# Optimization experiments

Measured on AMD Instinct MI355X. Metric: run time of the kernel, lower is better.

## Reference

```python
import jax, jax.numpy as jnp
import numpy as np

EPS = 1e-5  # F.layer_norm default eps
H_STEP = 0.1


def double_layer(x, K1, K2):
    # x: [1, Cin, N]; K1: [Cmid, Cin]; K2: [Cout, Cmid]  (1x1 conv1d == matmul)
    x = jnp.einsum('oc,bcn->bon', K1, x)
    # F.layer_norm(x, x.shape): normalize over the whole tensor, no affine
    m = jnp.mean(x)
    v = jnp.mean((x - m) ** 2)
    x = jnp.tanh((x - m) * jax.lax.rsqrt(v + EPS))
    return jnp.einsum('oc,bcn->bon', K2, x)


def setup_inputs() -> dict:
    key = jax.random.key(0)
    ks = jax.random.split(key, 12)
    N = 4096; nNin = 64; nopen = 256; nhid = 256; nNclose = 256
    nlayer = 8; num_output = 1024; E0 = 16 * N
    stdv = 1e-3
    return {
        'xn': jax.random.normal(ks[0], (1, nNin, N), jnp.float32),
        'K1Nopen': jax.random.normal(ks[1], (nopen, nNin), jnp.float32) * stdv,
        'K2Nopen': jax.random.normal(ks[2], (nopen, nopen), jnp.float32) * stdv,
        'KNclose': jax.random.normal(ks[3], (nNclose, nopen), jnp.float32) * stdv,
        'KN1': jax.random.uniform(ks[4], (nlayer, nhid, 2 * nopen), jnp.float32) * stdv,
        'KN2': jax.random.uniform(ks[5], (nlayer, nopen, nhid), jnp.float32) * stdv,
        'lin1_w': jax.random.normal(ks[6], (nopen, nopen), jnp.float32) / np.sqrt(nopen),
        'lin1_b': jnp.zeros((nopen,), jnp.float32),
        'lin2_w': jax.random.normal(ks[7], (num_output, nopen), jnp.float32) / np.sqrt(nopen),
        'lin2_b': jnp.zeros((num_output,), jnp.float32),
        'edge_i': jax.random.randint(ks[8], (E0,), 0, N),
        'edge_j': jax.random.randint(ks[9], (E0,), 0, N),
    }


def reference(xn, K1Nopen, K2Nopen, KNclose, KN1, KN2,
              lin1_w, lin1_b, lin2_w, lin2_b, edge_i, edge_j):
    N = xn.shape[-1]
    # gcn_norm's add_remaining_self_loops: input edge list has no self loops,
    # so append one per node once (fixed shapes; D[i,i] == exp(0) == 1 == fill).
    I = jnp.concatenate([edge_i, jnp.arange(N)])
    J = jnp.concatenate([edge_j, jnp.arange(N)])

    xn = double_layer(xn, K1Nopen, K2Nopen)  # [1, nopen, N]
    nlayers = KN1.shape[0]
    for i in range(nlayers):
        # --- updateGraph: dense pairwise Gaussian affinity, then gcn_norm ---
        f = xn[0]                          # [C, N]
        sq = jnp.sum(f * f, axis=0)        # [N]
        D = jax.nn.relu(sq[None, :] + sq[:, None] - 2.0 * (f.T @ f))  # [N, N]
        D = jnp.exp(-2.0 * (D / jnp.std(D, ddof=1)))
        w = D[I, J]                                          # gather edge affinities
        deg = jax.ops.segment_sum(w, J, num_segments=N)
        dis = jnp.where(deg > 0, jax.lax.rsqrt(deg), 0.0)
        W = dis[I] * w * dis[J]                              # normalized edge weights [E]
        # --- nodeLap = edgeDiv(nodeGrad(xn)) ---
        g = W[None, None, :] * (xn[:, :, I] - xn[:, :, J])   # nodeGrad [1, C, E]
        wg = (W[None, None, :] * g)[0].T                     # [E, C]
        lap = (jax.ops.segment_sum(wg, I, num_segments=N)
               - jax.ops.segment_sum(wg, J, num_segments=N)).T[None]  # [1, C, N]
        dxn = jnp.concatenate([xn, lap], axis=1)             # varlet features [1, 2C, N]
        dxn = double_layer(dxn, KN1[i], KN2[i])              # [1, C, N]
        xn = xn + H_STEP * dxn                               # heat update

    xn = jnp.einsum('oc,bcn->bon', KNclose, xn)[0].T         # [N, nNclose]
    x = jax.nn.elu(xn @ lin1_w.T + lin1_b)
    x = x @ lin2_w.T + lin2_b
    return jax.nn.log_softmax(x, axis=1)                     # [N, num_output]
```

## Files before the change

kernel.cpp:

```cpp
#include <hip/hip_runtime.h>
#include <hip/hip_bf16.h>

#define N_NODES 4096
#define CF      256
#define CIN     64
#define E0_EDGES 65536
#define NLAYER  8
#define NOUT    1024
#define CN      (CF * N_NODES)
#define STD_BLOCKS 64

typedef unsigned short ushort;
typedef __attribute__((ext_vector_type(8))) short s8v;
typedef __attribute__((ext_vector_type(4))) float f4v;

__device__ __forceinline__ ushort f2bf(float x){
  unsigned int u = __builtin_bit_cast(unsigned int, x);
  return (ushort)((u + 0x7FFFu + ((u >> 16) & 1u)) >> 16);
}
__device__ __forceinline__ float bf2f(ushort h){
  unsigned int u = ((unsigned int)h) << 16;
  return __builtin_bit_cast(float, u);
}

__device__ __forceinline__ float waveSumF(float v){
  #pragma unroll
  for (int o = 32; o; o >>= 1) v += __shfl_xor(v, o);
  return v;
}
__device__ __forceinline__ double waveSumD(double v){
  #pragma unroll
  for (int o = 32; o; o >>= 1) v += __shfl_xor(v, o);
  return v;
}
__device__ __forceinline__ float waveMaxF(float v){
  #pragma unroll
  for (int o = 32; o; o >>= 1) v = fmaxf(v, __shfl_xor(v, o));
  return v;
}
__device__ float blockSumF(float v){
  __shared__ float sm[4];
  v = waveSumF(v);
  int l = threadIdx.x & 63, w = threadIdx.x >> 6;
  __syncthreads();
  if (l == 0) sm[w] = v;
  __syncthreads();
  return sm[0] + sm[1] + sm[2] + sm[3];
}
__device__ double blockSumD(double v){
  __shared__ double sm[4];
  v = waveSumD(v);
  int l = threadIdx.x & 63, w = threadIdx.x >> 6;
  __syncthreads();
  if (l == 0) sm[w] = v;
  __syncthreads();
  return sm[0] + sm[1] + sm[2] + sm[3];
}
__device__ float blockMaxF(float v){
  __shared__ float sm[4];
  v = waveMaxF(v);
  int l = threadIdx.x & 63, w = threadIdx.x >> 6;
  __syncthreads();
  if (l == 0) sm[w] = v;
  __syncthreads();
  return fmaxf(fmaxf(sm[0], sm[1]), fmaxf(sm[2], sm[3]));
}

#define MF(a,b,c) c = __builtin_amdgcn_mfma_f32_16x16x32_bf16(a, b, c, 0, 0, 0)

template<int BK, int NT, int ACT, bool WF32, bool WBF, bool WFH, bool MV, bool TRI>
__global__ __launch_bounds__(256)
void gemmB1(const ushort* __restrict__ A1, const ushort* __restrict__ A2,
            int lda, int splitAt,
            const ushort* __restrict__ B, int ldb,
            float* __restrict__ Cf, ushort* __restrict__ Cb, ushort* __restrict__ Cfh,
            int ldc, size_t cStrideZ, int kChunk,
            float alpha, float beta, const float* __restrict__ bias,
            double* __restrict__ pS, double* __restrict__ pS2)
{
  constexpr int BR  = (NT == 64) ? 64 : 32;
  constexpr int NCA = BK / 32;
  constexpr int NCB = (NT == 64) ? BK / 32 : BK / 64;
  __shared__ ushort As[2][64][BK + 8], Bs[2][BR][BK + 8];
  const int tid = threadIdx.x;
  const int ar = tid >> 2, ak = (tid & 3) * (BK / 4);
  const int br = (NT == 64) ? (tid >> 2) : (tid >> 3);
  const int bk_ = (NT == 64) ? ak : (tid & 7) * (BK / 8);
  int bx = blockIdx.x, by = blockIdx.y;
  if (TRI) {
    const int trT[10] = {0,0,0,0,1,1,1,2,2,3};
    const int tcT[10] = {0,1,2,3,1,2,3,2,3,3};
    by = trT[blockIdx.x]; bx = tcT[blockIdx.x];
  }
  const int row0 = by * 64, col0 = bx * NT;
  const int kStart = blockIdx.z * kChunk;
  const int nT = kChunk / BK;

  const int wid = tid >> 6, lane = tid & 63;
  const int wr = (wid >> 1) * 32, wc = (wid & 1) * (NT / 2);
  const int fr = lane & 15, fk = (lane >> 4) * 8;

  f4v acc[2][NT / 32] = {};
  s8v rA0[NCA], rB0[NCB], rA1[NCA], rB1[NCB];

#define LOADTILE(T, RA, RB) { \
    int k0 = kStart + (T) * BK; \
    const ushort* Ag; int kk; \
    if (k0 < splitAt) { Ag = A1; kk = k0; } else { Ag = A2; kk = k0 - splitAt; } \
    size_t aoff = (size_t)(row0 + ar) * lda + kk + ak; \
    size_t boff = (size_t)(col0 + br) * ldb + k0 + bk_; \
    _Pragma("unroll") \
    for (int c = 0; c < NCA; c++) RA[c] = *(const s8v*)(Ag + aoff + 8 * c); \
    _Pragma("unroll") \
    for (int c = 0; c < NCB; c++) RB[c] = *(const s8v*)(B + boff + 8 * c); }

#define STORETILE(BUF, RA, RB) { \
    _Pragma("unroll") \
    for (int c = 0; c < NCA; c++) *(s8v*)&As[BUF][ar][ak + 8 * c] = RA[c]; \
    _Pragma("unroll") \
    for (int c = 0; c < NCB; c++) *(s8v*)&Bs[BUF][br][bk_ + 8 * c] = RB[c]; }

#define MFMAT(BUF) { \
    _Pragma("unroll") \
    for (int ks = 0; ks < BK; ks += 32) { \
      s8v a0 = *(const s8v*)&As[BUF][wr + fr][ks + fk]; \
      s8v a1 = *(const s8v*)&As[BUF][wr + 16 + fr][ks + fk]; \
      s8v b0 = *(const s8v*)&Bs[BUF][wc + fr][ks + fk]; \
      MF(a0, b0, acc[0][0]); \
      MF(a1, b0, acc[1][0]); \
      if constexpr (NT == 64) { \
        s8v b1 = *(const s8v*)&Bs[BUF][wc + 16 + fr][ks + fk]; \
        MF(a0, b1, acc[0][1]); \
        MF(a1, b1, acc[1][1]); } } }

  LOADTILE(0, rA0, rB0);
  if (nT > 1) LOADTILE(1, rA1, rB1);
  STORETILE(0, rA0, rB0);

  for (int t = 0; t < nT; t += 2) {
    __syncthreads();
    if (t + 2 < nT) LOADTILE(t + 2, rA0, rB0);
    MFMAT(0);
    if (t + 1 < nT) {
      STORETILE(1, rA1, rB1);
      __syncthreads();
      if (t + 3 < nT) LOADTILE(t + 3, rA1, rB1);
      MFMAT(1);
      if (t + 2 < nT) STORETILE(0, rA0, rB0);
    }
  }
#undef LOADTILE
#undef STORETILE
#undef MFMAT

  double s = 0, s2 = 0;
  #pragma unroll
  for (int m = 0; m < 2; m++)
    #pragma unroll
    for (int n = 0; n < NT / 32; n++) {
      const int rowb = row0 + wr + m * 16 + (lane >> 4) * 4;
      const int col  = col0 + wc + n * 16 + fr;
      ushort4 hv;
      #pragma unroll
      for (int q = 0; q < 4; q++) {
        size_t cidx = (size_t)(rowb + q) * ldc + col;
        float v = alpha * acc[m][n][q];
        if (cStrideZ) {
          Cf[blockIdx.z * cStrideZ + cidx] = v;
        } else {
          if (beta != 0.0f) v += beta * Cf[cidx];
          if (bias) v += bias[col];
          if (ACT == 1) v = (v > 0.0f) ? v : expm1f(v);
          if (WF32) Cf[cidx] = v;
          if (WBF)  Cb[cidx] = f2bf(v);
          if (WFH)  ((ushort*)&hv)[q] = f2bf(v);
          if (MV)   { s += v; s2 += (double)v * v; }
        }
      }
      if (WFH && !cStrideZ)
        *(ushort4*)(Cfh + (size_t)col * N_NODES + rowb) = hv;
    }
  if (MV) {
    s  = blockSumD(s);
    s2 = blockSumD(s2);
    if (tid == 0) {
      int bid = blockIdx.y * gridDim.x + blockIdx.x;
      pS[bid] = s; pS2[bid] = s2;
    }
  }
}

#define OFF_K1   0
#define OFF_K2   16384
#define OFF_KNC  81920
#define OFF_KN1  147456
#define OFF_KN2  1196032
#define OFF_L1   1720320
#define OFF_L2   1785856
#define NW_TOT   2048000

__global__ __launch_bounds__(256)
void prepWK(const float* s0, const float* s1, const float* s2, const float* s3,
            const float* s4, const float* s5, const float* s6,
            ushort* __restrict__ h)
{
  const int sizes[7] = {16384, 65536, 65536, 1048576, 524288, 65536, 262144};
  const int offs[7]  = {OFF_K1, OFF_K2, OFF_KNC, OFF_KN1, OFF_KN2, OFF_L1, OFF_L2};
  int seg = blockIdx.y;
  const float* src = seg==0?s0: seg==1?s1: seg==2?s2: seg==3?s3: seg==4?s4: seg==5?s5: s6;
  int n = sizes[seg], off = offs[seg];
  for (int i = blockIdx.x * 256 + threadIdx.x; i < n; i += gridDim.x * 256)
    h[off + i] = f2bf(src[i]);
}

__global__ __launch_bounds__(256)
void transposeBF(const float* __restrict__ in, ushort* __restrict__ outh, int R, int Cc)
{
  __shared__ float t[32][33];
  int x  = blockIdx.x * 32 + threadIdx.x;
  int y0 = blockIdx.y * 32;
  for (int dy = threadIdx.y; dy < 32; dy += 8)
    t[dy][threadIdx.x] = in[(size_t)(y0 + dy) * Cc + x];
  __syncthreads();
  int ox  = y0 + threadIdx.x;
  int oy0 = blockIdx.x * 32;
  for (int dy = threadIdx.y; dy < 32; dy += 8)
    outh[(size_t)(oy0 + dy) * R + ox] = f2bf(t[threadIdx.x][dy]);
}

__global__ __launch_bounds__(256)
void tanhNormBF(ushort* __restrict__ h, const double* __restrict__ pS,
                const double* __restrict__ pS2)
{
  __shared__ float bc[2];
  double a = pS[threadIdx.x] + pS[threadIdx.x + 256];
  double b = pS2[threadIdx.x] + pS2[threadIdx.x + 256];
  a = blockSumD(a);
  b = blockSumD(b);
  if (threadIdx.x == 0) {
    double m   = a / (double)CN;
    double var = b / (double)CN - m * m;
    bc[0] = (float)m;
    bc[1] = (float)(1.0 / sqrt(var + 1e-5));
  }
  __syncthreads();
  float mf = bc[0], rs = bc[1];
  for (size_t i = ((size_t)blockIdx.x * 256 + threadIdx.x) * 8; i < CN;
       i += (size_t)256 * 256 * 8) {
    s8v hv = *(s8v*)(h + i);
    #pragma unroll
    for (int k = 0; k < 8; k++) {
      float x = bf2f((ushort)hv[k]);
      x = tanhf((x - mf) * rs);
      hv[k] = (short)f2bf(x);
    }
    *(s8v*)(h + i) = hv;
  }
}

__global__ __launch_bounds__(256)
void sqSHK(const ushort* __restrict__ fTh, float* __restrict__ sq,
           float* __restrict__ sP, float* __restrict__ hP, float* __restrict__ deg)
{
  __shared__ float smS[4][256], smH[4][256];
  int b = blockIdx.x, w = threadIdx.x >> 6, lane = threadIdx.x & 63;
  if (threadIdx.x < 64) deg[b * 64 + threadIdx.x] = 0.0f;
  float sA[4] = {0,0,0,0}, hA[4] = {0,0,0,0};
  for (int rr = 0; rr < 16; rr++) {
    int n = b * 64 + rr * 4 + w;
    ushort4 u = ((const ushort4*)(fTh + (size_t)n * CF))[lane];
    float x0 = bf2f(u.x), x1 = bf2f(u.y), x2 = bf2f(u.z), x3 = bf2f(u.w);
    float q = waveSumF(x0*x0 + x1*x1 + x2*x2 + x3*x3);
    if (lane == 0) sq[n] = q;
    sA[0] += x0; sA[1] += x1; sA[2] += x2; sA[3] += x3;
    hA[0] += x0*q; hA[1] += x1*q; hA[2] += x2*q; hA[3] += x3*q;
  }
  #pragma unroll
  for (int k = 0; k < 4; k++) { smS[w][lane*4+k] = sA[k]; smH[w][lane*4+k] = hA[k]; }
  __syncthreads();
  int t = threadIdx.x;
  sP[(size_t)b * 256 + t] = smS[0][t] + smS[1][t] + smS[2][t] + smS[3][t];
  hP[(size_t)b * 256 + t] = smH[0][t] + smH[1][t] + smH[2][t] + smH[3][t];
}

__global__ __launch_bounds__(256)
void stdPartsK(const float* __restrict__ sP, const float* __restrict__ hP,
               const float* __restrict__ Gp, const float* __restrict__ sq,
               double* __restrict__ parts)
{
  int b = blockIdx.x, t = threadIdx.x;
  double S1 = 0, S2 = 0, sd = 0, hd = 0, gf = 0;
  for (int i = b * 256 + t; i < N_NODES; i += STD_BLOCKS * 256) {
    double q = sq[i]; S1 += q; S2 += q * q;
  }
  if (b == 0) {
    float sv = 0, hv = 0;
    for (int p = 0; p < 64; p++) { sv += sP[p * 256 + t]; hv += hP[p * 256 + t]; }
    sd = (double)sv * sv; hd = (double)hv * sv;
  }
  for (int i = b * 256 + t; i < CF * CF; i += STD_BLOCKS * 256) {
    int r = i >> 8, c = i & 255;
    if (r > c) continue;
    double g = 0;
    #pragma unroll 4
    for (int z = 0; z < 16; z++) g += Gp[(size_t)z * 65536 + i];
    gf += (r == c) ? g * g : 2.0 * g * g;
  }
  S1 = blockSumD(S1);
  S2 = blockSumD(S2);
  sd = blockSumD(sd);
  hd = blockSumD(hd);
  gf = blockSumD(gf);
  if (t == 0) {
    parts[0 * STD_BLOCKS + b] = S1;
    parts[1 * STD_BLOCKS + b] = S2;
    parts[2 * STD_BLOCKS + b] = sd;
    parts[3 * STD_BLOCKS + b] = hd;
    parts[4 * STD_BLOCKS + b] = gf;
  }
}

__global__ __launch_bounds__(256)
void edgeWK(const int* __restrict__ ei, const int* __restrict__ ej,
            const ushort* __restrict__ fTh, const float* __restrict__ sq,
            const double* __restrict__ parts, float* __restrict__ wE,
            float* __restrict__ deg)
{
  __shared__ float c0s;
  if (threadIdx.x < 64) {
    int l = threadIdx.x;
    double v0 = waveSumD(parts[0 * STD_BLOCKS + l]);
    double v1 = waveSumD(parts[1 * STD_BLOCKS + l]);
    double v2 = waveSumD(parts[2 * STD_BLOCKS + l]);
    double v3 = waveSumD(parts[3 * STD_BLOCKS + l]);
    double v4 = waveSumD(parts[4 * STD_BLOCKS + l]);
    if (l == 0) {
      double NN = (double)N_NODES;
      double sum1 = 2.0 * NN * v0 - 2.0 * v2;
      double sum2 = 2.0 * NN * v1 + 2.0 * v0 * v0 + 4.0 * v4 - 8.0 * v3;
      double n2 = NN * NN;
      double var = (sum2 - sum1 * sum1 / n2) / (n2 - 1.0);
      double sdev = sqrt(var > 0 ? var : 0);
      c0s = (float)(-2.0 / sdev);
    }
  }
  __syncthreads();
  float c0 = c0s;
  int w = threadIdx.x >> 6, lane = threadIdx.x & 63;
  int e0 = (blockIdx.x * 4 + w) * 4;
  for (int q = 0; q < 4; q++) {
    int e = e0 + q;
    int i = ei[e], j = ej[e];
    ushort4 ua = ((const ushort4*)(fTh + (size_t)i * CF))[lane];
    ushort4 ub = ((const ushort4*)(fTh + (size_t)j * CF))[lane];
    float d = waveSumF(bf2f(ua.x)*bf2f(ub.x) + bf2f(ua.y)*bf2f(ub.y) +
                       bf2f(ua.z)*bf2f(ub.z) + bf2f(ua.w)*bf2f(ub.w));
    if (lane == 0) {
      float dist = fmaxf(sq[i] + sq[j] - 2.0f * d, 0.0f);
      float ww = expf(c0 * dist);
      wE[e] = ww;
      unsafeAtomicAdd(&deg[j], ww);
    }
  }
}

__global__ __launch_bounds__(256)
void csrCountK(const int* __restrict__ ei, const int* __restrict__ ej,
               int* __restrict__ cntO, int* __restrict__ cntI)
{
  int e = blockIdx.x * 256 + threadIdx.x;
  atomicAdd(&cntO[ei[e]], 1);
  atomicAdd(&cntI[ej[e]], 1);
}

__global__ __launch_bounds__(256)
void csrScanK(const int* __restrict__ cntO, const int* __restrict__ cntI,
              int* __restrict__ ofsO, int* __restrict__ ofsI)
{
  __shared__ int smO[256], smI[256];
  int t = threadIdx.x;
  int lo[16], li[16];
  int sO = 0, sI = 0;
  #pragma unroll
  for (int k = 0; k < 16; k++) {
    lo[k] = cntO[t * 16 + k]; li[k] = cntI[t * 16 + k];
    sO += lo[k]; sI += li[k];
  }
  smO[t] = sO; smI[t] = sI;
  __syncthreads();
  for (int off = 1; off < 256; off <<= 1) {
    int aO = (t >= off) ? smO[t - off] : 0;
    int aI = (t >= off) ? smI[t - off] : 0;
    __syncthreads();
    smO[t] += aO; smI[t] += aI;
    __syncthreads();
  }
  int bO = smO[t] - sO;
  int bI = smI[t] - sI;
  #pragma unroll
  for (int k = 0; k < 16; k++) {
    ofsO[t * 16 + k] = bO; bO += lo[k];
    ofsI[t * 16 + k] = bI; bI += li[k];
  }
}

__global__ __launch_bounds__(256)
void csrFillK(const int* __restrict__ ei, const int* __restrict__ ej,
              const int* __restrict__ ofsO, const int* __restrict__ ofsI,
              int* __restrict__ curO, int* __restrict__ curI,
              int2* __restrict__ lstO, int2* __restrict__ lstI)
{
  int e = blockIdx.x * 256 + threadIdx.x;
  int i = ei[e], j = ej[e];
  int p = atomicAdd(&curO[i], 1); lstO[ofsO[i] + p] = make_int2(j, e);
  int q = atomicAdd(&curI[j], 1); lstI[ofsI[j] + q] = make_int2(i, e);
}

__global__ __launch_bounds__(256)
void gatherLapK(const int2* __restrict__ lstO, const int2* __restrict__ lstI,
                const int* __restrict__ ofsO, const int* __restrict__ ofsI,
                const int* __restrict__ cntO, const int* __restrict__ cntI,
                const float* __restrict__ wE, const float* __restrict__ deg,
                const ushort* __restrict__ fTh, ushort* __restrict__ lapTh)
{
  int w = threadIdx.x >> 6, lane = threadIdx.x & 63;
  int n = blockIdx.x * 4 + w;
  ushort4 u = ((const ushort4*)(fTh + (size_t)n * CF))[lane];
  float o0 = bf2f(u.x), o1 = bf2f(u.y), o2 = bf2f(u.z), o3 = bf2f(u.w);
  float dn = rsqrtf(1.0f + deg[n]);
  float a0 = 0, a1 = 0, a2 = 0, a3 = 0;
  int p0 = ofsO[n], pc = cntO[n];
  for (int k = 0; k < pc; k++) {
    int2 oe = lstO[p0 + k];
    float W = dn * wE[oe.y] * rsqrtf(1.0f + deg[oe.x]);
    float W2 = W * W;
    ushort4 v = ((const ushort4*)(fTh + (size_t)oe.x * CF))[lane];
    a0 += W2 * (o0 - bf2f(v.x)); a1 += W2 * (o1 - bf2f(v.y));
    a2 += W2 * (o2 - bf2f(v.z)); a3 += W2 * (o3 - bf2f(v.w));
  }
  int q0 = ofsI[n], qc = cntI[n];
  for (int k = 0; k < qc; k++) {
    int2 oe = lstI[q0 + k];
    float W = dn * wE[oe.y] * rsqrtf(1.0f + deg[oe.x]);
    float W2 = W * W;
    ushort4 v = ((const ushort4*)(fTh + (size_t)oe.x * CF))[lane];
    a0 += W2 * (o0 - bf2f(v.x)); a1 += W2 * (o1 - bf2f(v.y));
    a2 += W2 * (o2 - bf2f(v.z)); a3 += W2 * (o3 - bf2f(v.w));
  }
  ushort4 rv;
  rv.x = f2bf(a0); rv.y = f2bf(a1); rv.z = f2bf(a2); rv.w = f2bf(a3);
  ((ushort4*)(lapTh + (size_t)n * CF))[lane] = rv;
}

__global__ __launch_bounds__(256)
void logSoftmaxK(const float* __restrict__ logits, float* __restrict__ out)
{
  int n = blockIdx.x;
  const float* row = logits + (size_t)n * NOUT;
  float mx = -1e30f;
  for (int o = threadIdx.x; o < NOUT; o += 256) mx = fmaxf(mx, row[o]);
  mx = blockMaxF(mx);
  float se = 0;
  for (int o = threadIdx.x; o < NOUT; o += 256) se += expf(row[o] - mx);
  se = blockSumF(se);
  float lse = mx + logf(se);
  for (int o = threadIdx.x; o < NOUT; o += 256) out[(size_t)n * NOUT + o] = row[o] - lse;
}

extern "C" void kernel_launch(void* const* d_in, const int* in_sizes, int n_in,
                              void* d_out, int out_size, void* d_ws, size_t ws_size,
                              hipStream_t stream)
{
  (void)in_sizes; (void)n_in; (void)out_size; (void)ws_size;
  const float* x0      = (const float*)d_in[0];
  const float* K1      = (const float*)d_in[1];
  const float* K2      = (const float*)d_in[2];
  const float* KNclose = (const float*)d_in[3];
  const float* KN1     = (const float*)d_in[4];
  const float* KN2     = (const float*)d_in[5];
  const float* lin1w   = (const float*)d_in[6];
  const float* lin1b   = (const float*)d_in[7];
  const float* lin2w   = (const float*)d_in[8];
  const float* lin2b   = (const float*)d_in[9];
  const int*   ei      = (const int*)d_in[10];
  const int*   ej      = (const int*)d_in[11];
  float* out = (float*)d_out;

  float* base   = (float*)d_ws;
  float* fT     = base;
  float* logits = fT + (size_t)CN;
  float* Gp     = logits + 4 * (size_t)CN;
  float* sq     = Gp + (size_t)CN;
  float* deg    = sq + N_NODES;
  float* sP     = deg + N_NODES;
  float* hP     = sP + 64 * 256;
  float* wE     = hP + 64 * 256;
  double* pS    = (double*)(wE + E0_EDGES + 2);
  double* pS2   = pS + 512;
  double* parts = pS2 + 512;

  ushort* u0 = (ushort*)(((uintptr_t)(parts + 5 * STD_BLOCKS) + 15) & ~(uintptr_t)15);
  ushort* fTh   = u0;
  ushort* fh    = fTh + (size_t)CN;
  ushort* lapTh = fh + (size_t)CN;
  ushort* uTh   = lapTh + (size_t)CN;
  ushort* wH    = uTh + (size_t)CN;
  int* ib = (int*)(((uintptr_t)(wH + NW_TOT) + 15) & ~(uintptr_t)15);
  int*  cntO = ib;
  int*  cntI = cntO + N_NODES;
  int*  ofsO = cntI + N_NODES;
  int*  ofsI = ofsO + N_NODES;
  int*  curO = ofsI + N_NODES;
  int*  curI = curO + N_NODES;
  int2* lstO = (int2*)(curI + N_NODES);
  int2* lstI = lstO + E0_EDGES;

  prepWK<<<dim3(64, 7), 256, 0, stream>>>(K1, K2, KNclose, KN1, KN2, lin1w, lin2w, wH);
  hipMemsetAsync(cntO, 0, 6 * N_NODES * sizeof(int), stream);
  csrCountK<<<E0_EDGES/256, 256, 0, stream>>>(ei, ej, cntO, cntI);
  csrScanK<<<1, 256, 0, stream>>>(cntO, cntI, ofsO, ofsI);
  csrFillK<<<E0_EDGES/256, 256, 0, stream>>>(ei, ej, ofsO, ofsI, curO, curI, lstO, lstI);

  transposeBF<<<dim3(N_NODES/32, CIN/32), dim3(32, 8), 0, stream>>>(x0, fh, CIN, N_NODES);
  gemmB1<64,32,0,0,1,0,1,false><<<dim3(8,64,1), 256, 0, stream>>>(
      fh, fh, CIN, 1 << 30, wH + OFF_K1, CIN,
      nullptr, uTh, nullptr, CF, 0, CIN, 1.f, 0.f, nullptr, pS, pS2);
  tanhNormBF<<<256, 256, 0, stream>>>(uTh, pS, pS2);
  gemmB1<128,32,0,1,1,1,0,false><<<dim3(8,64,1), 256, 0, stream>>>(
      uTh, uTh, CF, 1 << 30, wH + OFF_K2, CF,
      fT, fTh, fh, CF, 0, CF, 1.f, 0.f, nullptr, nullptr, nullptr);

  for (int L = 0; L < NLAYER; L++) {
    const ushort* k1h = wH + OFF_KN1 + (size_t)L * CF * 2 * CF;
    const ushort* k2h = wH + OFF_KN2 + (size_t)L * CF * CF;

    sqSHK<<<64, 256, 0, stream>>>(fTh, sq, sP, hP, deg);
    gemmB1<128,64,0,1,0,0,0,true><<<dim3(10,1,16), 256, 0, stream>>>(
        fh, fh, N_NODES, 1 << 30, fh, N_NODES,
        Gp, nullptr, nullptr, CF, 65536, 256, 1.f, 0.f, nullptr, nullptr, nullptr);
    stdPartsK<<<STD_BLOCKS, 256, 0, stream>>>(sP, hP, Gp, sq, parts);
    edgeWK<<<E0_EDGES/16, 256, 0, stream>>>(ei, ej, fTh, sq, parts, wE, deg);
    gatherLapK<<<N_NODES/4, 256, 0, stream>>>(lstO, lstI, ofsO, ofsI, cntO, cntI,
                                              wE, deg, fTh, lapTh);
    gemmB1<128,32,0,0,1,0,1,false><<<dim3(8,64,1), 256, 0, stream>>>(
        fTh, lapTh, CF, 256, k1h, 2*CF,
        nullptr, uTh, nullptr, CF, 0, 2*CF, 1.f, 0.f, nullptr, pS, pS2);
    tanhNormBF<<<256, 256, 0, stream>>>(uTh, pS, pS2);
    gemmB1<128,32,0,1,1,1,0,false><<<dim3(8,64,1), 256, 0, stream>>>(
        uTh, uTh, CF, 1 << 30, k2h, CF,
        fT, fTh, fh, CF, 0, CF, 0.1f, 1.f, nullptr, nullptr, nullptr);
  }

  gemmB1<128,32,0,0,1,0,0,false><<<dim3(8,64,1), 256, 0, stream>>>(
      fTh, fTh, CF, 1 << 30, wH + OFF_KNC, CF,
      nullptr, uTh, nullptr, CF, 0, CF, 1.f, 0.f, nullptr, nullptr, nullptr);
  gemmB1<128,32,1,0,1,0,0,false><<<dim3(8,64,1), 256, 0, stream>>>(
      uTh, uTh, CF, 1 << 30, wH + OFF_L1, CF,
      nullptr, lapTh, nullptr, CF, 0, CF, 1.f, 0.f, lin1b, nullptr, nullptr);
  gemmB1<128,64,0,1,0,0,0,false><<<dim3(16,64,1), 256, 0, stream>>>(
      lapTh, lapTh, CF, 1 << 30, wH + OFF_L2, CF,
      logits, nullptr, nullptr, NOUT, 0, CF, 1.f, 0.f, lin2b, nullptr, nullptr);
  logSoftmaxK<<<N_NODES, 256, 0, stream>>>(logits, out);
}
```

Before: 805.9 us.

## Parametrize GEMM tile rows, use 32x32 tiles, fold sqSHK into Gram GEMM

```diff
diff --git a/kernel.cpp b/kernel.cpp
--- a/kernel.cpp
+++ b/kernel.cpp
@@ -68,7 +68,8 @@
 
 #define MF(a,b,c) c = __builtin_amdgcn_mfma_f32_16x16x32_bf16(a, b, c, 0, 0, 0)
 
-template<int BK, int NT, int ACT, bool WF32, bool WBF, bool WFH, bool MV, bool TRI>
+template<int BK, int MT, int NT, int ACT, bool WF32, bool WBF, bool WFH,
+         bool MV, bool TRI, bool SQSH>
 __global__ __launch_bounds__(256)
 void gemmB1(const ushort* __restrict__ A1, const ushort* __restrict__ A2,
             int lda, int splitAt,
@@ -76,31 +77,60 @@
             float* __restrict__ Cf, ushort* __restrict__ Cb, ushort* __restrict__ Cfh,
             int ldc, size_t cStrideZ, int kChunk,
             float alpha, float beta, const float* __restrict__ bias,
-            double* __restrict__ pS, double* __restrict__ pS2)
-{
-  constexpr int BR  = (NT == 64) ? 64 : 32;
-  constexpr int NCA = BK / 32;
-  constexpr int NCB = (NT == 64) ? BK / 32 : BK / 64;
-  __shared__ ushort As[2][64][BK + 8], Bs[2][BR][BK + 8];
+            double* __restrict__ pS, double* __restrict__ pS2,
+            const ushort* __restrict__ fThp, float* __restrict__ sqp,
+            float* __restrict__ sPp, float* __restrict__ hPp,
+            float* __restrict__ degp)
+{
+  constexpr int TPR_A = 256 / MT;
+  constexpr int TPR_B = 256 / NT;
+  constexpr int NCA = (MT * BK) / 2048;
+  constexpr int NCB = (NT * BK) / 2048;
+  constexpr int MR = MT / 32, NR = NT / 32;
+  __shared__ ushort As[2][MT][BK + 8], Bs[2][NT][BK + 8];
   const int tid = threadIdx.x;
-  const int ar = tid >> 2, ak = (tid & 3) * (BK / 4);
-  const int br = (NT == 64) ? (tid >> 2) : (tid >> 3);
-  const int bk_ = (NT == 64) ? ak : (tid & 7) * (BK / 8);
+  const int ar = tid / TPR_A, ak = (tid % TPR_A) * (NCA * 8);
+  const int br = tid / TPR_B, bk_ = (tid % TPR_B) * (NCB * 8);
   int bx = blockIdx.x, by = blockIdx.y;
   if (TRI) {
     const int trT[10] = {0,0,0,0,1,1,1,2,2,3};
     const int tcT[10] = {0,1,2,3,1,2,3,2,3,3};
     by = trT[blockIdx.x]; bx = tcT[blockIdx.x];
   }
-  const int row0 = by * 64, col0 = bx * NT;
+
+  if constexpr (SQSH) {
+    __shared__ float smS[4][256], smH[4][256];
+    int g = blockIdx.z * gridDim.x + blockIdx.x;
+    if (g < 64) {
+      int w = tid >> 6, ln = tid & 63;
+      if (tid < 64) degp[g * 64 + tid] = 0.0f;
+      float sA[4] = {0,0,0,0}, hA[4] = {0,0,0,0};
+      for (int rr = 0; rr < 16; rr++) {
+        int n = g * 64 + rr * 4 + w;
+        ushort4 u = ((const ushort4*)(fThp + (size_t)n * CF))[ln];
+        float x0 = bf2f(u.x), x1 = bf2f(u.y), x2 = bf2f(u.z), x3 = bf2f(u.w);
+        float q = waveSumF(x0*x0 + x1*x1 + x2*x2 + x3*x3);
+        if (ln == 0) sqp[n] = q;
+        sA[0] += x0; sA[1] += x1; sA[2] += x2; sA[3] += x3;
+        hA[0] += x0*q; hA[1] += x1*q; hA[2] += x2*q; hA[3] += x3*q;
+      }
+      #pragma unroll
+      for (int k = 0; k < 4; k++) { smS[w][ln*4+k] = sA[k]; smH[w][ln*4+k] = hA[k]; }
+      __syncthreads();
+      sPp[(size_t)g * 256 + tid] = smS[0][tid] + smS[1][tid] + smS[2][tid] + smS[3][tid];
+      hPp[(size_t)g * 256 + tid] = smH[0][tid] + smH[1][tid] + smH[2][tid] + smH[3][tid];
+    }
+  }
+
+  const int row0 = by * MT, col0 = bx * NT;
   const int kStart = blockIdx.z * kChunk;
   const int nT = kChunk / BK;
 
   const int wid = tid >> 6, lane = tid & 63;
-  const int wr = (wid >> 1) * 32, wc = (wid & 1) * (NT / 2);
+  const int wr = (wid >> 1) * (MT / 2), wc = (wid & 1) * (NT / 2);
   const int fr = lane & 15, fk = (lane >> 4) * 8;
 
-  f4v acc[2][NT / 32] = {};
+  f4v acc[MR][NR] = {};
   s8v rA0[NCA], rB0[NCB], rA1[NCA], rB1[NCB];
 
 #define LOADTILE(T, RA, RB) { \
@@ -123,15 +153,15 @@
 #define MFMAT(BUF) { \
     _Pragma("unroll") \
     for (int ks = 0; ks < BK; ks += 32) { \
-      s8v a0 = *(const s8v*)&As[BUF][wr + fr][ks + fk]; \
-      s8v a1 = *(const s8v*)&As[BUF][wr + 16 + fr][ks + fk]; \
-      s8v b0 = *(const s8v*)&Bs[BUF][wc + fr][ks + fk]; \
-      MF(a0, b0, acc[0][0]); \
-      MF(a1, b0, acc[1][0]); \
-      if constexpr (NT == 64) { \
-        s8v b1 = *(const s8v*)&Bs[BUF][wc + 16 + fr][ks + fk]; \
-        MF(a0, b1, acc[0][1]); \
-        MF(a1, b1, acc[1][1]); } } }
+      s8v a[MR], b[NR]; \
+      _Pragma("unroll") \
+      for (int m = 0; m < MR; m++) a[m] = *(const s8v*)&As[BUF][wr + m*16 + fr][ks + fk]; \
+      _Pragma("unroll") \
+      for (int n = 0; n < NR; n++) b[n] = *(const s8v*)&Bs[BUF][wc + n*16 + fr][ks + fk]; \
+      _Pragma("unroll") \
+      for (int m = 0; m < MR; m++) \
+        _Pragma("unroll") \
+        for (int n = 0; n < NR; n++) MF(a[m], b[n], acc[m][n]); } }
 
   LOADTILE(0, rA0, rB0);
   if (nT > 1) LOADTILE(1, rA1, rB1);
@@ -155,9 +185,9 @@
 
   double s = 0, s2 = 0;
   #pragma unroll
-  for (int m = 0; m < 2; m++)
+  for (int m = 0; m < MR; m++)
     #pragma unroll
-    for (int n = 0; n < NT / 32; n++) {
+    for (int n = 0; n < NR; n++) {
       const int rowb = row0 + wr + m * 16 + (lane >> 4) * 4;
       const int col  = col0 + wc + n * 16 + fr;
       ushort4 hv;
@@ -233,8 +263,10 @@
                 const double* __restrict__ pS2)
 {
   __shared__ float bc[2];
-  double a = pS[threadIdx.x] + pS[threadIdx.x + 256];
-  double b = pS2[threadIdx.x] + pS2[threadIdx.x + 256];
+  double a = pS[threadIdx.x] + pS[threadIdx.x + 256] +
+             pS[threadIdx.x + 512] + pS[threadIdx.x + 768];
+  double b = pS2[threadIdx.x] + pS2[threadIdx.x + 256] +
+             pS2[threadIdx.x + 512] + pS2[threadIdx.x + 768];
   a = blockSumD(a);
   b = blockSumD(b);
   if (threadIdx.x == 0) {
@@ -256,31 +288,6 @@
     }
     *(s8v*)(h + i) = hv;
   }
-}
-
-__global__ __launch_bounds__(256)
-void sqSHK(const ushort* __restrict__ fTh, float* __restrict__ sq,
-           float* __restrict__ sP, float* __restrict__ hP, float* __restrict__ deg)
-{
-  __shared__ float smS[4][256], smH[4][256];
-  int b = blockIdx.x, w = threadIdx.x >> 6, lane = threadIdx.x & 63;
-  if (threadIdx.x < 64) deg[b * 64 + threadIdx.x] = 0.0f;
-  float sA[4] = {0,0,0,0}, hA[4] = {0,0,0,0};
-  for (int rr = 0; rr < 16; rr++) {
-    int n = b * 64 + rr * 4 + w;
-    ushort4 u = ((const ushort4*)(fTh + (size_t)n * CF))[lane];
-    float x0 = bf2f(u.x), x1 = bf2f(u.y), x2 = bf2f(u.z), x3 = bf2f(u.w);
-    float q = waveSumF(x0*x0 + x1*x1 + x2*x2 + x3*x3);
-    if (lane == 0) sq[n] = q;
-    sA[0] += x0; sA[1] += x1; sA[2] += x2; sA[3] += x3;
-    hA[0] += x0*q; hA[1] += x1*q; hA[2] += x2*q; hA[3] += x3*q;
-  }
-  #pragma unroll
-  for (int k = 0; k < 4; k++) { smS[w][lane*4+k] = sA[k]; smH[w][lane*4+k] = hA[k]; }
-  __syncthreads();
-  int t = threadIdx.x;
-  sP[(size_t)b * 256 + t] = smS[0][t] + smS[1][t] + smS[2][t] + smS[3][t];
-  hP[(size_t)b * 256 + t] = smH[0][t] + smH[1][t] + smH[2][t] + smH[3][t];
 }
 
 __global__ __launch_bounds__(256)
@@ -496,8 +503,8 @@
   float* hP     = sP + 64 * 256;
   float* wE     = hP + 64 * 256;
   double* pS    = (double*)(wE + E0_EDGES + 2);
-  double* pS2   = pS + 512;
-  double* parts = pS2 + 512;
+  double* pS2   = pS + 1024;
+  double* parts = pS2 + 1024;
 
   ushort* u0 = (ushort*)(((uintptr_t)(parts + 5 * STD_BLOCKS) + 15) & ~(uintptr_t)15);
   ushort* fTh   = u0;
@@ -522,43 +529,50 @@
   csrFillK<<<E0_EDGES/256, 256, 0, stream>>>(ei, ej, ofsO, ofsI, curO, curI, lstO, lstI);
 
   transposeBF<<<dim3(N_NODES/32, CIN/32), dim3(32, 8), 0, stream>>>(x0, fh, CIN, N_NODES);
-  gemmB1<64,32,0,0,1,0,1,false><<<dim3(8,64,1), 256, 0, stream>>>(
+  gemmB1<64,32,32,0,0,1,0,1,false,false><<<dim3(8,128,1), 256, 0, stream>>>(
       fh, fh, CIN, 1 << 30, wH + OFF_K1, CIN,
-      nullptr, uTh, nullptr, CF, 0, CIN, 1.f, 0.f, nullptr, pS, pS2);
+      nullptr, uTh, nullptr, CF, 0, CIN, 1.f, 0.f, nullptr, pS, pS2,
+      nullptr, nullptr, nullptr, nullptr, nullptr);
   tanhNormBF<<<256, 256, 0, stream>>>(uTh, pS, pS2);
-  gemmB1<128,32,0,1,1,1,0,false><<<dim3(8,64,1), 256, 0, stream>>>(
+  gemmB1<128,32,32,0,1,1,1,0,false,false><<<dim3(8,128,1), 256, 0, stream>>>(
       uTh, uTh, CF, 1 << 30, wH + OFF_K2, CF,
-      fT, fTh, fh, CF, 0, CF, 1.f, 0.f, nullptr, nullptr, nullptr);
+      fT, fTh, fh, CF, 0, CF, 1.f, 0.f, nullptr, nullptr, nullptr,
+      nullptr, nullptr, nullptr, nullptr, nullptr);
 
   for (int L = 0; L < NLAYER; L++) {
     const ushort* k1h = wH + OFF_KN1 + (size_t)L * CF * 2 * CF;
     const ushort* k2h = wH + OFF_KN2 + (size_t)L * CF * CF;
 
-    sqSHK<<<64, 256, 0, stream>>>(fTh, sq, sP, hP, deg);
-    gemmB1<128,64,0,1,0,0,0,true><<<dim3(10,1,16), 256, 0, stream>>>(
+    gemmB1<128,64,64,0,1,0,0,0,true,true><<<dim3(10,1,16), 256, 0, stream>>>(
         fh, fh, N_NODES, 1 << 30, fh, N_NODES,
-        Gp, nullptr, nullptr, CF, 65536, 256, 1.f, 0.f, nullptr, nullptr, nullptr);
+        Gp, nullptr, nullptr, CF, 65536, 256, 1.f, 0.f, nullptr, nullptr, nullptr,
+        fTh, sq, sP, hP, deg);
     stdPartsK<<<STD_BLOCKS, 256, 0, stream>>>(sP, hP, Gp, sq, parts);
     edgeWK<<<E0_EDGES/16, 256, 0, stream>>>(ei, ej, fTh, sq, parts, wE, deg);
     gatherLapK<<<N_NODES/4, 256, 0, stream>>>(lstO, lstI, ofsO, ofsI, cntO, cntI,
                                               wE, deg, fTh, lapTh);
-    gemmB1<128,32,0,0,1,0,1,false><<<dim3(8,64,1), 256, 0, stream>>>(
+    gemmB1<128,32,32,0,0,1,0,1,false,false><<<dim3(8,128,1), 256, 0, stream>>>(
         fTh, lapTh, CF, 256, k1h, 2*CF,
-        nullptr, uTh, nullptr, CF, 0, 2*CF, 1.f, 0.f, nullptr, pS, pS2);
+        nullptr, uTh, nullptr, CF, 0, 2*CF, 1.f, 0.f, nullptr, pS, pS2,
+        nullptr, nullptr, nullptr, nullptr, nullptr);
     tanhNormBF<<<256, 256, 0, stream>>>(uTh, pS, pS2);
-    gemmB1<128,32,0,1,1,1,0,false><<<dim3(8,64,1), 256, 0, stream>>>(
+    gemmB1<128,32,32,0,1,1,1,0,false,false><<<dim3(8,128,1), 256, 0, stream>>>(
         uTh, uTh, CF, 1 << 30, k2h, CF,
-        fT, fTh, fh, CF, 0, CF, 0.1f, 1.f, nullptr, nullptr, nullptr);
-  }
-
-  gemmB1<128,32,0,0,1,0,0,false><<<dim3(8,64,1), 256, 0, stream>>>(
+        fT, fTh, fh, CF, 0, CF, 0.1f, 1.f, nullptr, nullptr, nullptr,
+        nullptr, nullptr, nullptr, nullptr, nullptr);
+  }
+
+  gemmB1<128,32,32,0,0,1,0,0,false,false><<<dim3(8,128,1), 256, 0, stream>>>(
       fTh, fTh, CF, 1 << 30, wH + OFF_KNC, CF,
-      nullptr, uTh, nullptr, CF, 0, CF, 1.f, 0.f, nullptr, nullptr, nullptr);
-  gemmB1<128,32,1,0,1,0,0,false><<<dim3(8,64,1), 256, 0, stream>>>(
+      nullptr, uTh, nullptr, CF, 0, CF, 1.f, 0.f, nullptr, nullptr, nullptr,
+      nullptr, nullptr, nullptr, nullptr, nullptr);
+  gemmB1<128,32,32,1,0,1,0,0,false,false><<<dim3(8,128,1), 256, 0, stream>>>(
       uTh, uTh, CF, 1 << 30, wH + OFF_L1, CF,
-      nullptr, lapTh, nullptr, CF, 0, CF, 1.f, 0.f, lin1b, nullptr, nullptr);
-  gemmB1<128,64,0,1,0,0,0,false><<<dim3(16,64,1), 256, 0, stream>>>(
+      nullptr, lapTh, nullptr, CF, 0, CF, 1.f, 0.f, lin1b, nullptr, nullptr,
+      nullptr, nullptr, nullptr, nullptr, nullptr);
+  gemmB1<128,64,64,0,1,0,0,0,false,false><<<dim3(16,64,1), 256, 0, stream>>>(
       lapTh, lapTh, CF, 1 << 30, wH + OFF_L2, CF,
-      logits, nullptr, nullptr, NOUT, 0, CF, 1.f, 0.f, lin2b, nullptr, nullptr);
+      logits, nullptr, nullptr, NOUT, 0, CF, 1.f, 0.f, lin2b, nullptr, nullptr,
+      nullptr, nullptr, nullptr, nullptr, nullptr);
   logSoftmaxK<<<N_NODES, 256, 0, stream>>>(logits, out);
 }
```

Result: faster. 780.0 us (-3.2%).
